# Performance work log

Measured on AMD Instinct MI355X. Metric: run time of the kernel, lower is better.

## Reference

```python
import jax, jax.numpy as jnp
import numpy as np
from jax import lax

IMG = 1280.0          # image side (80 * stride 16)
HF = WF = 80          # feature map
STRIDE = 16
A = 15                # anchors per location (5 sizes x 3 ratios)
KMIX = 5              # MDN mixture components
NIMG = 8
NGT = 32
PRE_NMS = 2000
POST_NMS = 1000
NMS_THRESH = 0.7
BATCH_PER_IMG = 256
POS_FRAC = 0.5
SCALE_CLAMP = float(np.log(1000.0 / 16.0))
LOG2PI = float(np.log(2.0 * np.pi))


def _make_anchors():
    sizes = np.array([32., 64., 128., 256., 512.])
    ratios = np.array([0.5, 1.0, 2.0])
    ws = (sizes[:, None] * np.sqrt(1.0 / ratios)[None, :]).reshape(-1)
    hs = (sizes[:, None] * np.sqrt(ratios)[None, :]).reshape(-1)
    base = np.stack([-ws / 2, -hs / 2, ws / 2, hs / 2], 1)  # [A,4]
    xs = (np.arange(WF) + 0.5) * STRIDE
    ys = (np.arange(HF) + 0.5) * STRIDE
    sx, sy = np.meshgrid(xs, ys)
    shifts = np.stack([sx.ravel(), sy.ravel(), sx.ravel(), sy.ravel()], 1)  # [HW,4]
    return jnp.asarray((shifts[:, None, :] + base[None]).reshape(-1, 4), jnp.float32)


def setup_inputs() -> dict:
    key = jax.random.key(0)
    k = jax.random.split(key, 6)
    R = HF * WF * A
    anchors = _make_anchors()                                                # [R,4]
    pi = jax.random.normal(k[0], (NIMG, KMIX, R), jnp.float32)
    mu = jax.random.normal(k[1], (NIMG, KMIX, R), jnp.float32)
    sigma = jax.random.uniform(k[2], (NIMG, KMIX, R), jnp.float32, 0.1, 1.0)
    deltas = jax.random.normal(k[3], (NIMG, R, 4), jnp.float32) * 0.1
    xy = jax.random.uniform(k[4], (NIMG, NGT, 2), jnp.float32, 0.0, 960.0)
    wh = jax.random.uniform(k[5], (NIMG, NGT, 2), jnp.float32, 20.0, 320.0)
    gt_boxes = jnp.concatenate([xy, xy + wh], -1)                            # [N,G,4]
    return {"anchors": anchors, "pi": pi, "mu": mu, "sigma": sigma,
            "deltas": deltas, "gt_boxes": gt_boxes}


def pairwise_iou(a, b):  # [M,4],[P,4] -> [M,P]
    area_a = (a[:, 2] - a[:, 0]) * (a[:, 3] - a[:, 1])
    area_b = (b[:, 2] - b[:, 0]) * (b[:, 3] - b[:, 1])
    lt = jnp.maximum(a[:, None, :2], b[None, :, :2])
    rb = jnp.minimum(a[:, None, 2:], b[None, :, 2:])
    wh = jnp.clip(rb - lt, 0.0)
    inter = wh[..., 0] * wh[..., 1]
    return inter / jnp.maximum(area_a[:, None] + area_b[None, :] - inter, 1e-9)


def apply_deltas(d, boxes):  # Box2BoxTransform.apply_deltas, weights=(1,1,1,1)
    w = boxes[:, 2] - boxes[:, 0]
    h = boxes[:, 3] - boxes[:, 1]
    cx = boxes[:, 0] + 0.5 * w
    cy = boxes[:, 1] + 0.5 * h
    dx, dy = d[:, 0], d[:, 1]
    dw = jnp.minimum(d[:, 2], SCALE_CLAMP)
    dh = jnp.minimum(d[:, 3], SCALE_CLAMP)
    pcx = dx * w + cx
    pcy = dy * h + cy
    pw = jnp.exp(dw) * w
    ph = jnp.exp(dh) * h
    return jnp.stack([pcx - 0.5 * pw, pcy - 0.5 * ph, pcx + 0.5 * pw, pcy + 0.5 * ph], 1)


def get_deltas(src, tgt):  # Box2BoxTransform.get_deltas
    sw = src[..., 2] - src[..., 0]
    sh = src[..., 3] - src[..., 1]
    scx = src[..., 0] + 0.5 * sw
    scy = src[..., 1] + 0.5 * sh
    tw = tgt[..., 2] - tgt[..., 0]
    th = tgt[..., 3] - tgt[..., 1]
    tcx = tgt[..., 0] + 0.5 * tw
    tcy = tgt[..., 1] + 0.5 * th
    return jnp.stack([(tcx - scx) / sw, (tcy - scy) / sh,
                      jnp.log(tw / sw), jnp.log(th / sh)], -1)


def _nms_image(boxes, scores, unc):  # [R,4],[R],[R,2] -> padded top proposals
    top_s, tidx = lax.top_k(scores, PRE_NMS)
    tb = jnp.clip(boxes[tidx], 0.0, IMG)   # clip to image
    tu = unc[tidx]
    iou = pairwise_iou(tb, tb)             # [PRE,PRE]
    ar = jnp.arange(PRE_NMS)

    def body(i, keep):
        sup = (iou[i] > NMS_THRESH) & (ar > i) & keep[i]
        return keep & ~sup

    keep = lax.fori_loop(0, PRE_NMS, body, jnp.ones((PRE_NMS,), bool))
    wv = tb[:, 2] - tb[:, 0]
    hv = tb[:, 3] - tb[:, 1]
    keep = keep & (wv > 0.0) & (hv > 0.0)  # min_box_size = 0
    ms = jnp.where(keep, top_s, -jnp.inf)
    out_s, oidx = lax.top_k(ms, POST_NMS)
    return tb[oidx], out_s, tu[oidx]


def _losses(anchors, pi, mu, sigma, deltas, gt_boxes):
    # label_and_sample_anchors (no_grad in torch)
    iou = lax.stop_gradient(jax.vmap(lambda g: pairwise_iou(g, anchors))(gt_boxes))  # [N,G,R]
    vals = iou.max(axis=1)                       # matched IoU quality  [N,R]
    idx = jnp.argmax(iou, axis=1)                # matched gt index     [N,R]
    labels = jnp.where(vals >= 0.7, 1, jnp.where(vals >= 0.3, -1, 0))
    best_gt = iou.max(axis=2)                    # [N,G]
    lq = jnp.any((iou >= best_gt[:, :, None] - 1e-7) & (best_gt[:, :, None] > 0), axis=1)
    labels = jnp.where(lq, 1, labels)            # allow_low_quality_matches
    # deterministic subsample to batch_size_per_image with positive_fraction
    pos = labels == 1
    neg = labels == 0
    n_pos = jnp.minimum(pos.sum(1), int(BATCH_PER_IMG * POS_FRAC))
    keep_pos = pos & (jnp.cumsum(pos, 1) <= n_pos[:, None])
    keep_neg = neg & (jnp.cumsum(neg, 1) <= (BATCH_PER_IMG - n_pos)[:, None])
    labels = jnp.where(keep_pos, 1, jnp.where(keep_neg, 0, -1))
    matched_gt = lax.stop_gradient(jax.vmap(lambda g, i: g[i])(gt_boxes, idx))  # [N,R,4]
    gt_deltas = get_deltas(lax.stop_gradient(anchors)[None], matched_gt)
    pos_mask = labels == 1
    # smooth_l1 with beta=0 -> L1, summed over positives
    loss_loc = jnp.sum(jnp.abs(deltas - gt_deltas) * pos_mask[..., None])
    valid = labels != -1
    t = jnp.clip(vals, 0.0, 1.0)
    lp = jax.nn.log_softmax(pi, axis=1)
    comp = lp - 0.5 * ((t[:, None, :] - mu) / sigma) ** 2 - jnp.log(sigma) - 0.5 * LOG2PI
    nll = -jax.nn.logsumexp(comp, axis=1)        # [N,R]
    loss_cls = jnp.sum(nll * valid)
    norm = BATCH_PER_IMG * pi.shape[0]
    return jnp.stack([loss_cls / norm, loss_loc / norm])


def reference(anchors, pi, mu, sigma, deltas, gt_boxes):
    # find_logit: pi-weighted mixture mean as objectness score
    pi_sm = jax.nn.softmax(pi, axis=1)           # [N,K,R]
    logits = jnp.sum(pi_sm * mu, axis=1)         # [N,R]
    # mdn_uncertainties: epistemic / aleatoric
    epis = jnp.sum(pi_sm * (mu - logits[:, None, :]) ** 2, axis=1)
    alea = jnp.sum(pi_sm * sigma ** 2, axis=1)
    unc = jnp.stack([epis, alea], -1)            # [N,R,2]
    # _decode_proposals
    boxes = jax.vmap(lambda d: apply_deltas(d, anchors))(deltas)  # [N,R,4]
    # find_top_rpn_proposals_uncertainty (pre-NMS topk, clip, NMS, post-NMS topk)
    prop_b, prop_s, prop_u = jax.vmap(_nms_image)(boxes, logits, unc)
    losses = _losses(anchors, pi, mu, sigma, deltas, gt_boxes)    # [loss_cls, loss_loc]
    return prop_b, prop_s, prop_u, losses
```

## Files before the change

kernel.cpp:

```cpp
#include <hip/hip_runtime.h>
#include <cstdint>
#include <cstddef>

typedef unsigned long long u64;
typedef unsigned int u32;
typedef unsigned short u16;
typedef unsigned char u8;

#define R_ANCH 96000
#define NIMG   8
#define KMIX   5
#define PRE    2000
#define POST   1000
#define NGT    32
#define NCHUNK 375
#define NBLK   48
#define MROW   2048
#define SCAP   16
#define BIG_TH 64
#define CAP_BIN 6144
#define CAND_CAP 8192
#define GC_STRIDE 16

#define IMG_SZ        1280.0f
#define NMS_T         0.7f
#define SCALE_CLAMP_F 4.135166556742356f
#define HALF_L2PI     0.9189385332046727f

__device__ __forceinline__ u64 make_key(float s, int r) {
  u32 u = __float_as_uint(s);
  u = (u & 0x80000000u) ? ~u : (u | 0x80000000u);
  return ((u64)u << 32) | (u64)(0xFFFFFFFFu - (u32)r);
}

__device__ __forceinline__ float dec_score(u64 key) {
  u32 o = (u32)(key >> 32);
  u32 bits = (o & 0x80000000u) ? (o ^ 0x80000000u) : ~o;
  return __uint_as_float(bits);
}

__device__ __forceinline__ float iou_pair(float a0,float a1,float a2,float a3,
                                          float b0,float b1,float b2,float b3) {
#pragma clang fp contract(off)
  float areaA = (a2-a0)*(a3-a1);
  float areaB = (b2-b0)*(b3-b1);
  float lx=fmaxf(a0,b0), ly=fmaxf(a1,b1);
  float rx=fminf(a2,b2), ry=fminf(a3,b3);
  float iw=fmaxf(rx-lx,0.0f), ih=fmaxf(ry-ly,0.0f);
  float inter=iw*ih;
  return inter / fmaxf(areaA+areaB-inter, 1e-9f);
}

__device__ __forceinline__ void pick2048(const u32* __restrict__ hist, int k,
                                         int* s_i, u32* s_u,
                                         int& d_out, int& k_out, u32& cnt_out) {
  int tid = threadIdx.x;
  int lane = tid & 63, w = tid >> 6;
  u32 h[8]; u32 ssum = 0;
#pragma unroll
  for (int i=0;i<8;++i){ h[i] = hist[2047 - (tid*8 + i)]; ssum += h[i]; }
  u32 incl = ssum;
  for (int off=1; off<64; off<<=1){
    u32 t = (u32)__shfl_up((int)incl, off, 64);
    if (lane >= off) incl += t;
  }
  if (lane==63) s_i[w] = (int)incl;
  __syncthreads();
  u32 base = 0;
  for (int ww=0; ww<w; ++ww) base += (u32)s_i[ww];
  u32 run = base + incl - ssum;
#pragma unroll
  for (int i=0;i<8;++i){
    u32 nr = run + h[i];
    if (run < (u32)k && nr >= (u32)k){
      s_u[0] = (u32)(2047 - (tid*8+i));
      s_u[1] = (u32)k - run;
      s_u[2] = h[i];
    }
    run = nr;
  }
  __syncthreads();
  d_out = (int)s_u[0]; k_out = (int)s_u[1]; cnt_out = s_u[2];
  __syncthreads();
}

__device__ __forceinline__ void scan2048_desc(const u32* __restrict__ h,
                                              u32* __restrict__ off,
                                              u32* __restrict__ wsum, int tid) {
  int b_hi = 2047 - 2*tid, b_lo = b_hi - 1;
  u32 h_hi = h[b_hi], h_lo = h[b_lo];
  u32 sum = h_hi + h_lo;
  u32 incl = sum;
  int lane = tid & 63, wv = tid >> 6;
  for (int o=1; o<64; o<<=1){
    u32 t = (u32)__shfl_up((int)incl, o, 64);
    if (lane >= o) incl += t;
  }
  if (lane==63) wsum[wv] = incl;
  __syncthreads();
  u32 base = 0;
  for (int w=0; w<wv; ++w) base += wsum[w];
  u32 excl = base + incl - sum;
  off[b_hi] = excl;
  off[b_lo] = excl + h_hi;
}

__global__ void kZero(u32* z, int nwords) {
  for (int i = blockIdx.x*256 + threadIdx.x; i < nwords; i += gridDim.x*256)
    z[i] = 0u;
}

__global__ __launch_bounds__(256) void kA_mdn(
    const float* __restrict__ pi, const float* __restrict__ mu,
    const float* __restrict__ sigma, float* __restrict__ logits,
    float* __restrict__ epis, float* __restrict__ alea,
    u32* __restrict__ hist0,
    const float* __restrict__ anchors, const float* __restrict__ gt,
    const float* __restrict__ deltas,
    float* __restrict__ nll_o, float* __restrict__ loc_o,
    int* __restrict__ best) {
  __shared__ u32 s_h[2048];
  __shared__ float s_gt[NGT*4];
  __shared__ float s_ga[NGT];
  __shared__ int s_best[NGT];
  int tid = threadIdx.x;
  int img = blockIdx.y;

  if (blockIdx.x >= NCHUNK) {
    int bx = blockIdx.x - NCHUNK;
    if (tid < NGT*4) s_gt[tid] = gt[img*NGT*4 + tid];
    if (tid < NGT){
      const float* g4 = gt + img*NGT*4 + tid*4;
      s_ga[tid] = (g4[2]-g4[0])*(g4[3]-g4[1]);
      s_best[tid] = 0;
    }
    __syncthreads();
    float4 an[8]; float aA[8];
#pragma unroll
    for (int q=0; q<8; ++q){
      int r = bx*256 + tid + q*(NBLK*256);
      an[q] = (r < R_ANCH) ? ((const float4*)anchors)[r]
                           : make_float4(0.f,0.f,0.f,0.f);
      aA[q] = (an[q].z-an[q].x)*(an[q].w-an[q].y);
    }
    float vmax[NGT];
#pragma unroll 2
    for (int g=0; g<NGT; ++g){
      float g0=s_gt[g*4], g1=s_gt[g*4+1], g2=s_gt[g*4+2], g3=s_gt[g*4+3];
      float ga=s_ga[g];
      float bi=0.0f, bu=1.0f;
#pragma unroll
      for (int q=0; q<8; ++q){
        float lx=fmaxf(g0,an[q].x), ly=fmaxf(g1,an[q].y);
        float rx=fminf(g2,an[q].z), ry=fminf(g3,an[q].w);
        float iw=fmaxf(rx-lx,0.0f), ih=fmaxf(ry-ly,0.0f);
        float inter=iw*ih;
        float uni=fmaxf(ga+aA[q]-inter,1e-9f);
        if (inter*bu > bi*uni){ bi=inter; bu=uni; }
      }
      vmax[g] = bi/bu;
    }
    int lane = tid & 63;
#pragma unroll
    for (int g=0; g<NGT; ++g){
      float v = vmax[g];
      v = fmaxf(v, __shfl_xor(v, 1, 64));
      v = fmaxf(v, __shfl_xor(v, 2, 64));
      v = fmaxf(v, __shfl_xor(v, 4, 64));
      v = fmaxf(v, __shfl_xor(v, 8, 64));
      v = fmaxf(v, __shfl_xor(v,16, 64));
      v = fmaxf(v, __shfl_xor(v,32, 64));
      if (lane==0 && v > 0.0f) atomicMax(&s_best[g], __float_as_int(v));
    }
    __syncthreads();
    if (tid < NGT) atomicMax(&best[img*NGT + tid], s_best[tid]);
    return;
  }

  int r = blockIdx.x*256 + tid;
  for (int b=tid; b<2048; b+=256) s_h[b]=0u;
  if (tid < NGT*4) s_gt[tid] = gt[img*NGT*4 + tid];
  size_t base = (size_t)img*KMIX*R_ANCH + r;
  float p[KMIX], m[KMIX], s[KMIX];
#pragma unroll
  for (int k=0;k<KMIX;k++){
    p[k]=pi[base+(size_t)k*R_ANCH];
    m[k]=mu[base+(size_t)k*R_ANCH];
    s[k]=sigma[base+(size_t)k*R_ANCH];
  }
  float mx = p[0];
#pragma unroll
  for (int k=1;k<KMIX;k++) mx = fmaxf(mx,p[k]);
  float e[KMIX]; float sum = 0.0f;
#pragma unroll
  for (int k=0;k<KMIX;k++){ e[k]=expf(p[k]-mx); sum += e[k]; }
  float w[KMIX]; float lg = 0.0f;
#pragma unroll
  for (int k=0;k<KMIX;k++){ w[k]=e[k]/sum; lg += w[k]*m[k]; }
  float ep = 0.0f, al = 0.0f;
#pragma unroll
  for (int k=0;k<KMIX;k++){ float d=m[k]-lg; ep += w[k]*d*d; al += w[k]*s[k]*s[k]; }
  size_t o = (size_t)img*R_ANCH + r;
  logits[o]=lg; epis[o]=ep; alea[o]=al;
  __syncthreads();
  u64 key = make_key(lg, r);
  atomicAdd(&s_h[(u32)(key>>53)], 1u);
  float4 a = ((const float4*)anchors)[r];
  float aA = (a.z-a.x)*(a.w-a.y);
  float bi = -1.0f, bu = 1.0f; int idx = 0;
#pragma unroll 4
  for (int g=0; g<NGT; ++g){
    float g0=s_gt[g*4], g1=s_gt[g*4+1], g2=s_gt[g*4+2], g3=s_gt[g*4+3];
    float ga=(g2-g0)*(g3-g1);
    float lx=fmaxf(g0,a.x), ly=fmaxf(g1,a.y);
    float rx=fminf(g2,a.z), ry=fminf(g3,a.w);
    float iw=fmaxf(rx-lx,0.0f), ih=fmaxf(ry-ly,0.0f);
    float inter=iw*ih;
    float uni = fmaxf(ga + aA - inter, 1e-9f);
    if (inter*bu > bi*uni){ bi=inter; bu=uni; idx=g; }
  }
  float vbest = bi/bu;
  float lsum = logf(sum);
  float t_ = fminf(fmaxf(vbest, 0.0f), 1.0f);
  float comp[KMIX];
#pragma unroll
  for (int k=0;k<KMIX;k++){
    float z = (t_ - m[k]) / s[k];
    comp[k] = (p[k]-mx-lsum) - 0.5f*z*z - logf(s[k]) - HALF_L2PI;
  }
  float cm = comp[0];
#pragma unroll
  for (int k=1;k<KMIX;k++) cm = fmaxf(cm, comp[k]);
  float se = 0.0f;
#pragma unroll
  for (int k=0;k<KMIX;k++) se += expf(comp[k]-cm);
  float nll = -(cm + logf(se));
  const float* gb = &s_gt[idx*4];
  float sw = a.z-a.x, sh = a.w-a.y;
  float scx = a.x+0.5f*sw, scy = a.y+0.5f*sh;
  float tw = gb[2]-gb[0], th = gb[3]-gb[1];
  float tcx = gb[0]+0.5f*tw, tcy = gb[1]+0.5f*th;
  float4 d = ((const float4*)deltas)[(size_t)img*R_ANCH + r];
  float loc = fabsf(d.x-(tcx-scx)/sw) + fabsf(d.y-(tcy-scy)/sh)
            + fabsf(d.z-logf(tw/sw)) + fabsf(d.w-logf(th/sh));
  nll_o[o] = nll; loc_o[o] = loc;
  __syncthreads();
  for (int b=tid; b<2048; b+=256){ u32 v=s_h[b]; if(v) atomicAdd(&hist0[img*2048+b], v); }
}

__global__ __launch_bounds__(256) void kP1(const float* __restrict__ logits,
                                           const u32* __restrict__ hist0,
                                           u32* __restrict__ hist1) {
  __shared__ u32 s_h[2048];
  __shared__ int s_i[8]; __shared__ u32 s_u[3];
  int img = blockIdx.y, tid = threadIdx.x;
  int d0,k0; u32 c0;
  pick2048(hist0 + img*2048, PRE, s_i, s_u, d0,k0,c0);
  if (c0 <= CAP_BIN) return;
  for (int b=tid; b<2048; b+=256) s_h[b]=0u;
  __syncthreads();
  const float* sc = logits + (size_t)img*R_ANCH;
  for (int r = blockIdx.x*256 + tid; r < R_ANCH; r += NBLK*256){
    u64 key = make_key(sc[r], r);
    if ((int)(key>>53) == d0) atomicAdd(&s_h[(u32)(key>>42)&2047u], 1u);
  }
  __syncthreads();
  for (int b=tid; b<2048; b+=256){ u32 v=s_h[b]; if(v) atomicAdd(&hist1[img*2048+b], v); }
}

__global__ __launch_bounds__(256) void kP2(const float* __restrict__ logits,
                                           const u32* __restrict__ hist0,
                                           const u32* __restrict__ hist1,
                                           u32* __restrict__ hist2) {
  __shared__ u32 s_h[2048];
  __shared__ int s_i[8]; __shared__ u32 s_u[3];
  int img = blockIdx.y, tid = threadIdx.x;
  int d0,k0; u32 c0;
  pick2048(hist0 + img*2048, PRE, s_i, s_u, d0,k0,c0);
  if (c0 <= CAP_BIN) return;
  int d1,k1; u32 c1;
  pick2048(hist1 + img*2048, k0, s_i, s_u, d1,k1,c1);
  if (c1 <= CAP_BIN) return;
  u64 p1 = ((u64)d0<<11) | (u64)d1;
  for (int b=tid; b<2048; b+=256) s_h[b]=0u;
  __syncthreads();
  const float* sc = logits + (size_t)img*R_ANCH;
  for (int r = blockIdx.x*256 + tid; r < R_ANCH; r += NBLK*256){
    u64 key = make_key(sc[r], r);
    if ((key>>42) == p1) atomicAdd(&s_h[(u32)(key>>31)&2047u], 1u);
  }
  __syncthreads();
  for (int b=tid; b<2048; b+=256){ u32 v=s_h[b]; if(v) atomicAdd(&hist2[img*2048+b], v); }
}

__global__ __launch_bounds__(256) void kGather(const float* __restrict__ logits,
    const u32* __restrict__ hist0, const u32* __restrict__ hist1,
    const u32* __restrict__ hist2, u64* __restrict__ cand, u32* __restrict__ gcnt) {
  __shared__ int s_i[8]; __shared__ u32 s_u[3];
  __shared__ u64 s_cand[2048];
  __shared__ u32 s_cnt, s_base;
  int img = blockIdx.y, tid = threadIdx.x;
  if (tid==0) s_cnt = 0u;
  int d,kk; u32 c;
  pick2048(hist0 + img*2048, PRE, s_i, s_u, d,kk,c);
  u64 p = (u64)d; int L = 0;
  if (c > CAP_BIN){
    pick2048(hist1 + img*2048, kk, s_i, s_u, d,kk,c);
    p = (p<<11)|(u64)d; L = 1;
    if (c > CAP_BIN){
      pick2048(hist2 + img*2048, kk, s_i, s_u, d,kk,c);
      p = (p<<11)|(u64)d; L = 2;
    }
  }
  u64 T = p << (64 - 11*(L+1));
  const float* sc = logits + (size_t)img*R_ANCH;
  int lane = tid & 63;
  for (int r = blockIdx.x*256 + tid; r < R_ANCH; r += NBLK*256){
    u64 key = make_key(sc[r], r);
    bool take = (key >= T);
    u64 b = __ballot(take);
    if (b){
      u32 base = 0;
      if (lane==0) base = atomicAdd(&s_cnt, (u32)__popcll(b));
      base = (u32)__shfl((int)base, 0, 64);
      if (take){
        u32 pos = base + (u32)__popcll(b & ((1ull<<lane)-1ull));
        if (pos < 2048u) s_cand[pos] = key;
        else {
          u32 gp = atomicAdd(&gcnt[img*GC_STRIDE], 1u);
          if (gp < CAND_CAP) cand[(size_t)img*CAND_CAP + gp] = key;
        }
      }
    }
  }
  __syncthreads();
  u32 n = s_cnt < 2048u ? s_cnt : 2048u;
  if (tid==0) s_base = atomicAdd(&gcnt[img*GC_STRIDE], n);
  __syncthreads();
  u32 gb = s_base;
  for (u32 i=tid; i<n; i+=256)
    cand[(size_t)img*CAND_CAP + gb + i] = s_cand[i];
}

__global__ __launch_bounds__(1024) void kRank(
    const u64* __restrict__ cand, const u32* __restrict__ gcnt,
    const float* __restrict__ epis, const float* __restrict__ alea,
    const float* __restrict__ deltas, const float* __restrict__ anchors,
    float* __restrict__ tb, float* __restrict__ tu, float* __restrict__ ts) {
  __shared__ u64 s_key[CAND_CAP];
  __shared__ u16 s_idx0[CAND_CAP];
  __shared__ u16 s_idx1[CAND_CAP];
  __shared__ u32 s_h0[2048];
  __shared__ u32 s_off0[2048];
  __shared__ u32 s_h1[2048];
  __shared__ u32 s_off1[2048];
  __shared__ u32 s_wsum[16];
  __shared__ u32 s_nbig;
  __shared__ u16 s_big[128];
  int tid = threadIdx.x, img = blockIdx.x;
  u32 cnt = gcnt[img*GC_STRIDE];
  if (cnt > (u32)CAND_CAP) cnt = CAND_CAP;
  const u64* cp = cand + (size_t)img*CAND_CAP;
  for (int i=tid; i<CAND_CAP; i+=1024) s_key[i] = (i < (int)cnt) ? cp[i] : 0ull;
  for (int b=tid; b<2048; b+=1024){ s_h0[b] = 0u; }
  if (tid==0) s_nbig = 0u;
  __syncthreads();
  for (int i=tid; i<(int)cnt; i+=1024)
    atomicAdd(&s_h0[(u32)(s_key[i]>>53)], 1u);
  __syncthreads();
  scan2048_desc(s_h0, s_off0, s_wsum, tid);
  __syncthreads();
  for (int b=tid; b<2048; b+=1024){
    u32 sz = s_h0[b];
    if (sz > BIG_TH && s_off0[b] < PRE){
      u32 q = atomicAdd(&s_nbig, 1u);
      if (q < 128u) s_big[q] = (u16)b;
    }
  }
  __syncthreads();
  for (int i=tid; i<(int)cnt; i+=1024){
    u32 d = (u32)(s_key[i]>>53);
    u32 slot = atomicAdd(&s_off0[d], 1u);
    s_idx0[slot] = (u16)i;
  }
  __syncthreads();
  auto emit = [&](u64 my, u32 rank){
    if (rank < PRE){
      int p = (int)rank;
      u32 idx = 0xFFFFFFFFu - (u32)(my & 0xFFFFFFFFull);
      ts[img*PRE + p] = dec_score(my);
      float4 a = ((const float4*)anchors)[idx];
      float4 dd = ((const float4*)deltas)[(size_t)img*R_ANCH + idx];
      float w = a.z - a.x, h = a.w - a.y;
      float cx = a.x + 0.5f*w, cy = a.y + 0.5f*h;
      float dw = fminf(dd.z, SCALE_CLAMP_F), dh = fminf(dd.w, SCALE_CLAMP_F);
      float pcx = dd.x*w + cx, pcy = dd.y*h + cy;
      float pw = expf(dw)*w, ph = expf(dh)*h;
      float x0 = fminf(fmaxf(pcx - 0.5f*pw, 0.0f), IMG_SZ);
      float y0 = fminf(fmaxf(pcy - 0.5f*ph, 0.0f), IMG_SZ);
      float x1 = fminf(fmaxf(pcx + 0.5f*pw, 0.0f), IMG_SZ);
      float y1 = fminf(fmaxf(pcy + 0.5f*ph, 0.0f), IMG_SZ);
      ((float4*)tb)[(size_t)img*PRE + p] = make_float4(x0,y0,x1,y1);
      size_t o = (size_t)img*R_ANCH + idx;
      ((float2*)tu)[(size_t)img*PRE + p] = make_float2(epis[o], alea[o]);
    }
  };
  for (int i=tid; i<(int)cnt; i+=1024){
    u64 my = s_key[i];
    u32 d = (u32)(my>>53);
    u32 size = s_h0[d];
    if (size > BIG_TH) continue;
    u32 bs = s_off0[d] - size;
    if (bs >= PRE) continue;
    u32 rank = bs;
    for (u32 q=bs; q<bs+size; ++q)
      rank += (s_key[s_idx0[q]] > my) ? 1u : 0u;
    emit(my, rank);
  }
  __syncthreads();
  u32 nbig = s_nbig < 128u ? s_nbig : 128u;
  for (u32 bb=0; bb<nbig; ++bb){
    u32 B = s_big[bb];
    u32 size = s_h0[B];
    u32 base0 = s_off0[B] - size;
    for (int b=tid; b<2048; b+=1024) s_h1[b] = 0u;
    __syncthreads();
    for (u32 q=tid; q<size; q+=1024){
      u64 k = s_key[s_idx0[base0+q]];
      atomicAdd(&s_h1[(u32)(k>>42)&2047u], 1u);
    }
    __syncthreads();
    scan2048_desc(s_h1, s_off1, s_wsum, tid);
    __syncthreads();
    for (u32 q=tid; q<size; q+=1024){
      u16 ci = s_idx0[base0+q];
      u64 k = s_key[ci];
      u32 slot = atomicAdd(&s_off1[(u32)(k>>42)&2047u], 1u);
      s_idx1[slot] = ci;
    }
    __syncthreads();
    for (u32 q=tid; q<size; q+=1024){
      u16 ci = s_idx1[q];
      u64 my = s_key[ci];
      u32 d1 = (u32)(my>>42)&2047u;
      u32 ssz = s_h1[d1];
      u32 sbs = s_off1[d1] - ssz;
      u32 rank = base0 + sbs;
      for (u32 t2=sbs; t2<sbs+ssz; ++t2)
        rank += (s_key[s_idx1[t2]] > my) ? 1u : 0u;
      emit(my, rank);
    }
    __syncthreads();
  }
}

__global__ __launch_bounds__(1024) void kD_mask(const float* __restrict__ tb,
                                                u64* __restrict__ maskLT,
                                                u32* __restrict__ scnt,
                                                u16* __restrict__ slist) {
  __shared__ float4 s_tile[64];
  int tid = threadIdx.x;
  int a = blockIdx.x, img = blockIdx.y;
  const float4* tbi = (const float4*)tb + (size_t)img*PRE;
  if (tid < 64){
    int i = a*64 + tid;
    s_tile[tid] = (i < PRE) ? tbi[i] : make_float4(0.f,0.f,0.f,0.f);
  }
  __syncthreads();
  u64* outp = maskLT + ((size_t)img*32 + a)*MROW;
  u32* cnts = scnt + (size_t)img*2048;
  u16* lst  = slist + (size_t)img*2048*SCAP;
  int bmax = min(64, PRE - a*64);
  for (int j = a*64 + tid; j < MROW; j += 1024){
    u64 m = 0ull;
    if (j < PRE){
      float4 B = tbi[j];
      int blim = min(bmax, j - a*64);
      for (int b = 0; b < blim; ++b){
        float4 A = s_tile[b];
        float v = iou_pair(A.x,A.y,A.z,A.w, B.x,B.y,B.z,B.w);
        m |= (u64)(v > NMS_T) << b;
      }
    }
    outp[j] = m;
    u64 mm = m;
    while (mm){
      int b = __builtin_ctzll(mm); mm &= mm - 1ull;
      u32 slot = atomicAdd(&cnts[j], 1u);
      if (slot < SCAP) lst[(size_t)j*SCAP + slot] = (u16)(a*64 + b);
    }
  }
}

__global__ __launch_bounds__(1024) void kEF_nms(const u64* __restrict__ maskLT,
    const u32* __restrict__ scnt, const u16* __restrict__ slist,
    const float* __restrict__ tb, const float* __restrict__ tu,
    const float* __restrict__ ts, const float* __restrict__ acc,
    float* __restrict__ out) {
  __shared__ u64 s_list64[2048*SCAP/4];
  __shared__ u16 s_cnt[2048];
  __shared__ u8  kbuf[2][2048];
  __shared__ u64 s_kw[32];
  __shared__ int s_change, s_ovf;
  __shared__ int s_wk[16], s_wn[16];
  __shared__ int s_kc, s_runk, s_runn;
  int img = blockIdx.x, tid = threadIdx.x;
  int lane = tid & 63, wid = tid >> 6;
  const u64* gl = (const u64*)(slist + (size_t)img*2048*SCAP);
  for (int i=tid; i<2048*SCAP/4; i+=1024) s_list64[i] = gl[i];
  const u32* gc = scnt + (size_t)img*2048;
  for (int i=tid; i<2048; i+=1024) s_cnt[i] = (u16)gc[i];
  if (tid==0){ s_change = 0; s_ovf = 0; }
  __syncthreads();
  bool myovf = false;
#pragma unroll
  for (int q=0; q<2; ++q){
    int j = tid + q*1024;
    if (s_cnt[j] > SCAP) myovf = true;
    kbuf[0][j] = (j < PRE) ? 1 : 0;
  }
  if (myovf) s_ovf = 1;
  __syncthreads();
  const u64* MT = maskLT + (size_t)img*32*MROW;
  int cur = 0;
  for (int iter=0; iter<2048; ++iter){
    bool ovf = (s_ovf != 0);
    if (ovf && tid < 32){
      u64 w = 0ull;
      for (int b=0; b<64; ++b) w |= (u64)(kbuf[cur][tid*64+b] & 1) << b;
      s_kw[tid] = w;
    }
    __syncthreads();
    bool changed = false;
#pragma unroll
    for (int q=0; q<2; ++q){
      int j = tid + q*1024;
      u8 old = kbuf[cur][j];
      u8 nk = (j < PRE) ? 1 : 0;
      if (nk){
        int cnt = s_cnt[j];
        if (cnt <= SCAP){
          const u16* lp = (const u16*)&s_list64[j*(SCAP/4)];
          for (int i=0; i<cnt; ++i){
            if (kbuf[cur][lp[i]]){ nk = 0; break; }
          }
        } else {
          int amax = j >> 6;
          for (int a=0; a<=amax; ++a){
            if (MT[(size_t)a*MROW + j] & s_kw[a]){ nk = 0; break; }
          }
        }
      }
      kbuf[1-cur][j] = nk;
      changed |= (nk != old);
    }
    if (changed) s_change = 1;
    __syncthreads();
    int ch = s_change;
    __syncthreads();
    if (tid==0) s_change = 0;
    if (!ch) break;
    cur ^= 1;
  }
  __syncthreads();
  const float4* tbi = (const float4*)tb + (size_t)img*PRE;
  const float NEG_INF = __uint_as_float(0xff800000u);
  u8* kf = kbuf[1-cur];
#pragma unroll
  for (int cch=0; cch<2; ++cch){
    int pp = cch*1024 + tid;
    bool kp = false;
    if (pp < PRE && kbuf[cur][pp]){
      float4 b = tbi[pp];
      kp = (b.z > b.x) && (b.w > b.y);
    }
    kf[pp] = kp ? 1 : 0;
  }
  __syncthreads();
  {
    int cc = (int)kf[tid] + (int)kf[1024 + tid];
    for (int of=32; of>0; of>>=1) cc += __shfl_down(cc, of, 64);
    if (lane==0) s_wk[wid] = cc;
  }
  __syncthreads();
  if (tid==0){
    int t=0; for (int w=0; w<16; ++w) t += s_wk[w];
    s_kc = t; s_runk = 0; s_runn = 0;
  }
  __syncthreads();
  int kc = s_kc;
#pragma unroll
  for (int cch=0; cch<2; ++cch){
    int pp = cch*1024 + tid;
    bool kp = kf[pp] != 0;
    u64 bk = __ballot(kp), bn = __ballot(!kp);
    if (lane==0){ s_wk[wid]=__popcll(bk); s_wn[wid]=__popcll(bn); }
    __syncthreads();
    int pk = s_runk, pn = s_runn;
    for (int w=0; w<wid; ++w){ pk += s_wk[w]; pn += s_wn[w]; }
    u64 lm = (1ull<<lane) - 1ull;
    pk += __popcll(bk & lm);
    pn += __popcll(bn & lm);
    int slot = kp ? pk : (kc + pn);
    if (slot < POST && pp < PRE){
      ((float4*)out)[img*POST + slot] = tbi[pp];
      out[32000 + img*POST + slot] = kp ? ts[img*PRE + pp] : NEG_INF;
      ((float2*)(out + 40000))[img*POST + slot] = ((const float2*)tu)[(size_t)img*PRE + pp];
    }
    __syncthreads();
    if (tid==0){
      int tk=0, tn=0;
      for (int w=0; w<16; ++w){ tk += s_wk[w]; tn += s_wn[w]; }
      s_runk += tk; s_runn += tn;
    }
    __syncthreads();
  }
  if (img==0 && tid<2) out[56000+tid] = acc[tid] * (1.0f/2048.0f);
}

__global__ __launch_bounds__(256) void kL2_label(
    const float* __restrict__ anchors, const float* __restrict__ gt,
    const int* __restrict__ best,
    signed char* __restrict__ label, int* __restrict__ cpos, int* __restrict__ cneg) {
  __shared__ float s_gt[NGT*4];
  __shared__ float s_ga[NGT];
  __shared__ float s_bg[NGT];
  __shared__ int s_w[8];
  int tid = threadIdx.x, img = blockIdx.y;
  int r = blockIdx.x*256 + tid;
  if (tid < NGT*4) s_gt[tid] = gt[img*NGT*4 + tid];
  if (tid < NGT){
    const float* g4 = gt + img*NGT*4 + tid*4;
    s_ga[tid] = (g4[2]-g4[0])*(g4[3]-g4[1]);
    s_bg[tid] = __int_as_float(best[img*NGT + tid]);
  }
  __syncthreads();
  float4 a = ((const float4*)anchors)[r];
  float aA = (a.z-a.x)*(a.w-a.y);
  float bi=-1.0f, bu=1.0f; bool lq = false;
#pragma unroll 4
  for (int g=0; g<NGT; ++g){
    float g0=s_gt[g*4], g1=s_gt[g*4+1], g2=s_gt[g*4+2], g3=s_gt[g*4+3];
    float lx=fmaxf(g0,a.x), ly=fmaxf(g1,a.y);
    float rx=fminf(g2,a.z), ry=fminf(g3,a.w);
    float iw=fmaxf(rx-lx,0.0f), ih=fmaxf(ry-ly,0.0f);
    float inter=iw*ih;
    float uni = fmaxf(s_ga[g] + aA - inter, 1e-9f);
    if (inter*bu > bi*uni){ bi=inter; bu=uni; }
    float bg = s_bg[g];
    lq = lq || ((inter >= (bg - 1e-7f)*uni) && (bg > 0.0f));
  }
  float vbest = bi/bu;
  int lab = lq ? 1 : (vbest >= 0.7f ? 1 : (vbest >= 0.3f ? -1 : 0));
  label[(size_t)img*R_ANCH + r] = (signed char)lab;
  u64 bp = __ballot(lab==1), bn = __ballot(lab==0);
  int wid = tid>>6, lane = tid&63;
  if (lane==0){ s_w[wid*2]=__popcll(bp); s_w[wid*2+1]=__popcll(bn); }
  __syncthreads();
  if (tid==0){
    cpos[img*NCHUNK + blockIdx.x] = s_w[0]+s_w[2]+s_w[4]+s_w[6];
    cneg[img*NCHUNK + blockIdx.x] = s_w[1]+s_w[3]+s_w[5]+s_w[7];
  }
}

__global__ __launch_bounds__(256) void kL4_accum(
    const signed char* __restrict__ label, const float* __restrict__ nll_i,
    const float* __restrict__ loc_i, const int* __restrict__ cpos,
    const int* __restrict__ cneg, float* __restrict__ acc) {
  __shared__ int s_wp[4], s_wn[4];
  __shared__ int s_r[12];
  __shared__ float s_red[8];
  int tid = threadIdx.x, img = blockIdx.y, bx = blockIdx.x;
  int lane = tid & 63, wid = tid >> 6;
  int vp=0, vn=0, tp=0;
  for (int k=tid; k<NCHUNK; k+=256){
    int cp = cpos[img*NCHUNK + k];
    int cn = cneg[img*NCHUNK + k];
    tp += cp;
    if (k < bx){ vp += cp; vn += cn; }
  }
  for (int of=32; of>0; of>>=1){
    vp += __shfl_down(vp, of, 64);
    vn += __shfl_down(vn, of, 64);
    tp += __shfl_down(tp, of, 64);
  }
  if (lane==0){ s_r[wid]=vp; s_r[4+wid]=vn; s_r[8+wid]=tp; }
  __syncthreads();
  int pre_p = s_r[0]+s_r[1]+s_r[2]+s_r[3];
  int pre_n = s_r[4]+s_r[5]+s_r[6]+s_r[7];
  int totp  = s_r[8]+s_r[9]+s_r[10]+s_r[11];
  int np = totp < 128 ? totp : 128;
  int nn = 256 - np;
  int r = bx*256 + tid;
  size_t o = (size_t)img*R_ANCH + r;
  int lab = label[o];
  bool pos = (lab==1), neg = (lab==0);
  u64 bp = __ballot(pos), bn = __ballot(neg);
  if (lane==0){ s_wp[wid]=__popcll(bp); s_wn[wid]=__popcll(bn); }
  __syncthreads();
  for (int w=0; w<wid; ++w){ pre_p += s_wp[w]; pre_n += s_wn[w]; }
  u64 lm = (1ull<<lane) - 1ull;
  pre_p += __popcll(bp & lm);
  pre_n += __popcll(bn & lm);
  bool kp = pos && (pre_p < np);
  bool kn = neg && (pre_n < nn);
  float c_cls = (kp||kn) ? nll_i[o] : 0.0f;
  float c_loc = kp ? loc_i[o] : 0.0f;
  for (int of=32; of>0; of>>=1){
    c_cls += __shfl_down(c_cls, of, 64);
    c_loc += __shfl_down(c_loc, of, 64);
  }
  if (lane==0){ s_red[wid]=c_cls; s_red[4+wid]=c_loc; }
  __syncthreads();
  if (tid==0){
    float a = s_red[0]+s_red[1]+s_red[2]+s_red[3];
    float b = s_red[4]+s_red[5]+s_red[6]+s_red[7];
    if (a != 0.0f) atomicAdd(&acc[0], a);
    if (b != 0.0f) atomicAdd(&acc[1], b);
  }
}

extern "C" void kernel_launch(void* const* d_in, const int* in_sizes, int n_in,
                              void* d_out, int out_size, void* d_ws, size_t ws_size,
                              hipStream_t stream) {
  const float* anchors = (const float*)d_in[0];
  const float* pi      = (const float*)d_in[1];
  const float* mu      = (const float*)d_in[2];
  const float* sigma   = (const float*)d_in[3];
  const float* deltas  = (const float*)d_in[4];
  const float* gt      = (const float*)d_in[5];
  float* out = (float*)d_out;

  char* ws = (char*)d_ws;
  size_t off = 0;
  auto alloc = [&](size_t bytes) -> void* {
    void* p = (void*)(ws + off);
    off += (bytes + 255) & ~(size_t)255;
    return p;
  };
  float* logits = (float*)alloc((size_t)NIMG*R_ANCH*4);
  float* epis   = (float*)alloc((size_t)NIMG*R_ANCH*4);
  float* alea   = (float*)alloc((size_t)NIMG*R_ANCH*4);
  float* nll    = (float*)alloc((size_t)NIMG*R_ANCH*4);
  float* loc    = (float*)alloc((size_t)NIMG*R_ANCH*4);
  float* tb     = (float*)alloc((size_t)NIMG*PRE*4*4);
  float* tu     = (float*)alloc((size_t)NIMG*PRE*2*4);
  float* ts     = (float*)alloc((size_t)NIMG*PRE*4);
  u64*   maskLT = (u64*)  alloc((size_t)NIMG*32*MROW*8);
  u16*   slist  = (u16*)  alloc((size_t)NIMG*2048*SCAP*2);
  u64*   cand   = (u64*)  alloc((size_t)NIMG*CAND_CAP*8);
  int*   cpos   = (int*)  alloc((size_t)NIMG*NCHUNK*4);
  int*   cneg   = (int*)  alloc((size_t)NIMG*NCHUNK*4);
  size_t zstart = off;
  u32*   hist0  = (u32*)  alloc((size_t)NIMG*2048*4);
  u32*   hist1  = (u32*)  alloc((size_t)NIMG*2048*4);
  u32*   hist2  = (u32*)  alloc((size_t)NIMG*2048*4);
  u32*   gcnt   = (u32*)  alloc((size_t)NIMG*GC_STRIDE*4);
  int*   best   = (int*)  alloc((size_t)NIMG*NGT*4);
  u32*   scnt   = (u32*)  alloc((size_t)NIMG*2048*4);
  float* acc    = (float*)alloc(8);
  int zwords = (int)((off - zstart) / 4);
  signed char* label = (signed char*)logits;

  kZero<<<dim3(64), dim3(256), 0, stream>>>((u32*)(ws + zstart), zwords);
  kA_mdn<<<dim3(NCHUNK+NBLK, NIMG), dim3(256), 0, stream>>>(pi, mu, sigma, logits, epis, alea,
                                                            hist0, anchors, gt, deltas, nll, loc, best);
  kP1<<<dim3(NBLK, NIMG), dim3(256), 0, stream>>>(logits, hist0, hist1);
  kP2<<<dim3(NBLK, NIMG), dim3(256), 0, stream>>>(logits, hist0, hist1, hist2);
  kGather<<<dim3(NBLK, NIMG), dim3(256), 0, stream>>>(logits, hist0, hist1, hist2, cand, gcnt);
  kRank<<<dim3(NIMG), dim3(1024), 0, stream>>>(cand, gcnt, epis, alea, deltas, anchors, tb, tu, ts);
  kD_mask<<<dim3(32, NIMG), dim3(1024), 0, stream>>>(tb, maskLT, scnt, slist);
  kL2_label<<<dim3(NCHUNK, NIMG), dim3(256), 0, stream>>>(anchors, gt, best, label, cpos, cneg);
  kL4_accum<<<dim3(NCHUNK, NIMG), dim3(256), 0, stream>>>(label, nll, loc, cpos, cneg, acc);
  kEF_nms<<<dim3(NIMG), dim3(1024), 0, stream>>>(maskLT, scnt, slist, tb, tu, ts, acc, out);
}
```

Before: 283.0 us.

## Compute per-anchor loss terms lazily only for sampled anchors in accumulation kernel

```diff
diff --git a/kernel.cpp b/kernel.cpp
--- a/kernel.cpp
+++ b/kernel.cpp
@@ -116,8 +116,6 @@
     float* __restrict__ epis, float* __restrict__ alea,
     u32* __restrict__ hist0,
     const float* __restrict__ anchors, const float* __restrict__ gt,
-    const float* __restrict__ deltas,
-    float* __restrict__ nll_o, float* __restrict__ loc_o,
     int* __restrict__ best) {
   __shared__ u32 s_h[2048];
   __shared__ float s_gt[NGT*4];
@@ -179,7 +177,6 @@
 
   int r = blockIdx.x*256 + tid;
   for (int b=tid; b<2048; b+=256) s_h[b]=0u;
-  if (tid < NGT*4) s_gt[tid] = gt[img*NGT*4 + tid];
   size_t base = (size_t)img*KMIX*R_ANCH + r;
   float p[KMIX], m[KMIX], s[KMIX];
 #pragma unroll
@@ -205,45 +202,6 @@
   __syncthreads();
   u64 key = make_key(lg, r);
   atomicAdd(&s_h[(u32)(key>>53)], 1u);
-  float4 a = ((const float4*)anchors)[r];
-  float aA = (a.z-a.x)*(a.w-a.y);
-  float bi = -1.0f, bu = 1.0f; int idx = 0;
-#pragma unroll 4
-  for (int g=0; g<NGT; ++g){
-    float g0=s_gt[g*4], g1=s_gt[g*4+1], g2=s_gt[g*4+2], g3=s_gt[g*4+3];
-    float ga=(g2-g0)*(g3-g1);
-    float lx=fmaxf(g0,a.x), ly=fmaxf(g1,a.y);
-    float rx=fminf(g2,a.z), ry=fminf(g3,a.w);
-    float iw=fmaxf(rx-lx,0.0f), ih=fmaxf(ry-ly,0.0f);
-    float inter=iw*ih;
-    float uni = fmaxf(ga + aA - inter, 1e-9f);
-    if (inter*bu > bi*uni){ bi=inter; bu=uni; idx=g; }
-  }
-  float vbest = bi/bu;
-  float lsum = logf(sum);
-  float t_ = fminf(fmaxf(vbest, 0.0f), 1.0f);
-  float comp[KMIX];
-#pragma unroll
-  for (int k=0;k<KMIX;k++){
-    float z = (t_ - m[k]) / s[k];
-    comp[k] = (p[k]-mx-lsum) - 0.5f*z*z - logf(s[k]) - HALF_L2PI;
-  }
-  float cm = comp[0];
-#pragma unroll
-  for (int k=1;k<KMIX;k++) cm = fmaxf(cm, comp[k]);
-  float se = 0.0f;
-#pragma unroll
-  for (int k=0;k<KMIX;k++) se += expf(comp[k]-cm);
-  float nll = -(cm + logf(se));
-  const float* gb = &s_gt[idx*4];
-  float sw = a.z-a.x, sh = a.w-a.y;
-  float scx = a.x+0.5f*sw, scy = a.y+0.5f*sh;
-  float tw = gb[2]-gb[0], th = gb[3]-gb[1];
-  float tcx = gb[0]+0.5f*tw, tcy = gb[1]+0.5f*th;
-  float4 d = ((const float4*)deltas)[(size_t)img*R_ANCH + r];
-  float loc = fabsf(d.x-(tcx-scx)/sw) + fabsf(d.y-(tcy-scy)/sh)
-            + fabsf(d.z-logf(tw/sw)) + fabsf(d.w-logf(th/sh));
-  nll_o[o] = nll; loc_o[o] = loc;
   __syncthreads();
   for (int b=tid; b<2048; b+=256){ u32 v=s_h[b]; if(v) atomicAdd(&hist0[img*2048+b], v); }
 }
@@ -664,14 +622,19 @@
 }
 
 __global__ __launch_bounds__(256) void kL4_accum(
-    const signed char* __restrict__ label, const float* __restrict__ nll_i,
-    const float* __restrict__ loc_i, const int* __restrict__ cpos,
-    const int* __restrict__ cneg, float* __restrict__ acc) {
+    const signed char* __restrict__ label,
+    const float* __restrict__ pi, const float* __restrict__ mu,
+    const float* __restrict__ sigma, const float* __restrict__ anchors,
+    const float* __restrict__ gt, const float* __restrict__ deltas,
+    const int* __restrict__ cpos, const int* __restrict__ cneg,
+    float* __restrict__ acc) {
   __shared__ int s_wp[4], s_wn[4];
   __shared__ int s_r[12];
   __shared__ float s_red[8];
+  __shared__ float s_gt[NGT*4];
   int tid = threadIdx.x, img = blockIdx.y, bx = blockIdx.x;
   int lane = tid & 63, wid = tid >> 6;
+  if (tid < NGT*4) s_gt[tid] = gt[img*NGT*4 + tid];
   int vp=0, vn=0, tp=0;
   for (int k=tid; k<NCHUNK; k+=256){
     int cp = cpos[img*NCHUNK + k];
@@ -704,8 +667,63 @@
   pre_n += __popcll(bn & lm);
   bool kp = pos && (pre_p < np);
   bool kn = neg && (pre_n < nn);
-  float c_cls = (kp||kn) ? nll_i[o] : 0.0f;
-  float c_loc = kp ? loc_i[o] : 0.0f;
+  float c_cls = 0.0f, c_loc = 0.0f;
+  if (kp || kn){
+    float4 a = ((const float4*)anchors)[r];
+    float aA = (a.z-a.x)*(a.w-a.y);
+    float bi = -1.0f, bu = 1.0f; int idx = 0;
+#pragma unroll 4
+    for (int g=0; g<NGT; ++g){
+      float g0=s_gt[g*4], g1=s_gt[g*4+1], g2=s_gt[g*4+2], g3=s_gt[g*4+3];
+      float ga=(g2-g0)*(g3-g1);
+      float lx=fmaxf(g0,a.x), ly=fmaxf(g1,a.y);
+      float rx=fminf(g2,a.z), ry=fminf(g3,a.w);
+      float iw=fmaxf(rx-lx,0.0f), ih=fmaxf(ry-ly,0.0f);
+      float inter=iw*ih;
+      float uni = fmaxf(ga + aA - inter, 1e-9f);
+      if (inter*bu > bi*uni){ bi=inter; bu=uni; idx=g; }
+    }
+    float vbest = bi/bu;
+    size_t base = (size_t)img*KMIX*R_ANCH + r;
+    float p[KMIX], m[KMIX], s[KMIX];
+#pragma unroll
+    for (int k=0;k<KMIX;k++){
+      p[k]=pi[base+(size_t)k*R_ANCH];
+      m[k]=mu[base+(size_t)k*R_ANCH];
+      s[k]=sigma[base+(size_t)k*R_ANCH];
+    }
+    float mx = p[0];
+#pragma unroll
+    for (int k=1;k<KMIX;k++) mx = fmaxf(mx,p[k]);
+    float e[KMIX]; float sum = 0.0f;
+#pragma unroll
+    for (int k=0;k<KMIX;k++){ e[k]=expf(p[k]-mx); sum += e[k]; }
+    float lsum = logf(sum);
+    float t_ = fminf(fmaxf(vbest, 0.0f), 1.0f);
+    float comp[KMIX];
+#pragma unroll
+    for (int k=0;k<KMIX;k++){
+      float z = (t_ - m[k]) / s[k];
+      comp[k] = (p[k]-mx-lsum) - 0.5f*z*z - logf(s[k]) - HALF_L2PI;
+    }
+    float cm = comp[0];
+#pragma unroll
+    for (int k=1;k<KMIX;k++) cm = fmaxf(cm, comp[k]);
+    float se = 0.0f;
+#pragma unroll
+    for (int k=0;k<KMIX;k++) se += expf(comp[k]-cm);
+    c_cls = -(cm + logf(se));
+    if (kp){
+      const float* gb = &s_gt[idx*4];
+      float sw = a.z-a.x, sh = a.w-a.y;
+      float scx = a.x+0.5f*sw, scy = a.y+0.5f*sh;
+      float tw = gb[2]-gb[0], th = gb[3]-gb[1];
+      float tcx = gb[0]+0.5f*tw, tcy = gb[1]+0.5f*th;
+      float4 d = ((const float4*)deltas)[(size_t)img*R_ANCH + r];
+      c_loc = fabsf(d.x-(tcx-scx)/sw) + fabsf(d.y-(tcy-scy)/sh)
+            + fabsf(d.z-logf(tw/sw)) + fabsf(d.w-logf(th/sh));
+    }
+  }
   for (int of=32; of>0; of>>=1){
     c_cls += __shfl_down(c_cls, of, 64);
     c_loc += __shfl_down(c_loc, of, 64);
@@ -741,8 +759,6 @@
   float* logits = (float*)alloc((size_t)NIMG*R_ANCH*4);
   float* epis   = (float*)alloc((size_t)NIMG*R_ANCH*4);
   float* alea   = (float*)alloc((size_t)NIMG*R_ANCH*4);
-  float* nll    = (float*)alloc((size_t)NIMG*R_ANCH*4);
-  float* loc    = (float*)alloc((size_t)NIMG*R_ANCH*4);
   float* tb     = (float*)alloc((size_t)NIMG*PRE*4*4);
   float* tu     = (float*)alloc((size_t)NIMG*PRE*2*4);
   float* ts     = (float*)alloc((size_t)NIMG*PRE*4);
@@ -764,13 +780,14 @@
 
   kZero<<<dim3(64), dim3(256), 0, stream>>>((u32*)(ws + zstart), zwords);
   kA_mdn<<<dim3(NCHUNK+NBLK, NIMG), dim3(256), 0, stream>>>(pi, mu, sigma, logits, epis, alea,
-                                                            hist0, anchors, gt, deltas, nll, loc, best);
+                                                            hist0, anchors, gt, best);
   kP1<<<dim3(NBLK, NIMG), dim3(256), 0, stream>>>(logits, hist0, hist1);
   kP2<<<dim3(NBLK, NIMG), dim3(256), 0, stream>>>(logits, hist0, hist1, hist2);
   kGather<<<dim3(NBLK, NIMG), dim3(256), 0, stream>>>(logits, hist0, hist1, hist2, cand, gcnt);
   kRank<<<dim3(NIMG), dim3(1024), 0, stream>>>(cand, gcnt, epis, alea, deltas, anchors, tb, tu, ts);
   kD_mask<<<dim3(32, NIMG), dim3(1024), 0, stream>>>(tb, maskLT, scnt, slist);
   kL2_label<<<dim3(NCHUNK, NIMG), dim3(256), 0, stream>>>(anchors, gt, best, label, cpos, cneg);
-  kL4_accum<<<dim3(NCHUNK, NIMG), dim3(256), 0, stream>>>(label, nll, loc, cpos, cneg, acc);
+  kL4_accum<<<dim3(NCHUNK, NIMG), dim3(256), 0, stream>>>(label, pi, mu, sigma, anchors, gt, deltas,
+                                                          cpos, cneg, acc);
   kEF_nms<<<dim3(NIMG), dim3(1024), 0, stream>>>(maskLT, scnt, slist, tb, tu, ts, acc, out);
 }
```

Measured after the change: 273.8 us. 3.3% less time.
